# Kernel optimization log

Hardware: AMD Instinct MI355X
Metric: run time of the kernel (lower is better)

## Reference

```python
import jax, jax.numpy as jnp
import numpy as np

D_MODEL = 1024
NHEAD = 16
HEAD_DIM = D_MODEL // NHEAD
ROPE_BASE = 10000.0


def _rope_freq(T, head_dim):
    half = head_dim // 2
    pos = jnp.arange(T, dtype=jnp.float32)
    idx = jnp.arange(half, dtype=jnp.float32)
    freq_div = ROPE_BASE ** (2.0 * idx / head_dim)
    return pos[:, None] / freq_div[None, :]  # [T, half]


def _rope_rotate(x, cos, sin):
    # x: [B, H, T, d]; cos/sin: [T, d//2]
    half = x.shape[-1] // 2
    xl, xr = x[..., :half], x[..., half:]
    c = cos[None, None]
    s = sin[None, None]
    return jnp.concatenate([xl * c - xr * s, xl * s + xr * c], axis=-1)


def setup_inputs() -> dict:
    key = jax.random.key(0)
    ks = jax.random.split(key, 12)
    B, T = 2, 2048
    sd = 1.0 / np.sqrt(D_MODEL)
    inp = {
        "query": jax.random.normal(ks[0], (B, T, D_MODEL), jnp.float32),
        "key": jax.random.normal(ks[1], (B, T, D_MODEL), jnp.float32),
        "value": jax.random.normal(ks[2], (B, T, D_MODEL), jnp.float32),
        "frac": jax.random.uniform(ks[3], (B, T), jnp.float32),
        # Linear weights stored [in, out] (torch W.T)
        "Wq": jax.random.normal(ks[4], (D_MODEL, D_MODEL), jnp.float32) * sd,
        "Wk": jax.random.normal(ks[5], (D_MODEL, D_MODEL), jnp.float32) * sd,
        "Wv": jax.random.normal(ks[6], (D_MODEL, D_MODEL), jnp.float32) * sd,
        "Wo": jax.random.normal(ks[7], (D_MODEL, D_MODEL), jnp.float32) * sd,
        "bq": jnp.zeros((D_MODEL,), jnp.float32),
        "bk": jnp.zeros((D_MODEL,), jnp.float32),
        "bv": jnp.zeros((D_MODEL,), jnp.float32),
        "bo": jnp.zeros((D_MODEL,), jnp.float32),
        "alpha_pos": jax.random.normal(ks[8], (NHEAD,), jnp.float32) * 0.1,
        "alpha_neg": jax.random.normal(ks[9], (NHEAD,), jnp.float32) * 0.1,
    }
    return inp


def reference(query, key, value, frac, Wq, Wk, Wv, Wo, bq, bk, bv, bo, alpha_pos, alpha_neg):
    B, T, dm = query.shape
    H, hd = NHEAD, HEAD_DIM
    scale = hd ** -0.5

    def split_heads(x):  # [B,T,dm] -> [B,H,T,hd]
        return x.reshape(B, T, H, hd).transpose(0, 2, 1, 3)

    Q = split_heads(query @ Wq + bq)
    K = split_heads(key @ Wk + bk)
    V = split_heads(value @ Wv + bv)

    freq = _rope_freq(T, hd)
    cos, sin = jnp.cos(freq), jnp.sin(freq)
    Q = _rope_rotate(Q, cos, sin)
    K = _rope_rotate(K, cos, sin)

    scores = jnp.einsum("bhqd,bhkd->bhqk", Q, K) * scale  # [B,H,T,T]

    # data-dependent stoichiometric bias
    D = frac[:, None, :] - frac[:, :, None]  # [B,T,T], D[b,i,j] = frac_j - frac_i
    D_pos = jax.nn.relu(D)
    D_neg = -jax.nn.relu(-D)
    bias = (alpha_pos[None, :, None, None] * D_pos[:, None] +
            alpha_neg[None, :, None, None] * D_neg[:, None])  # [B,H,T,T]
    scores = scores + bias

    probs = jax.nn.softmax(scores, axis=-1)
    out = jnp.einsum("bhqk,bhkd->bhqd", probs, V)  # [B,H,T,hd]
    out = out.transpose(0, 2, 1, 3).reshape(B, T, dm)
    return out @ Wo + bo
```

## Files before the change

kernel.cpp:

```cpp
#include <hip/hip_runtime.h>


typedef unsigned short u16;
typedef __bf16 bf8v __attribute__((ext_vector_type(8)));
typedef __bf16 bf4v __attribute__((ext_vector_type(4)));
typedef float f32x4 __attribute__((ext_vector_type(4)));

#define D_MODEL 1024
#define T_SEQ   2048
#define NHEAD   16
#define HDIM    64
#define BATCH   2
#define M_TOT   (BATCH * T_SEQ)
#define LOG2E   1.4426950408889634f

__device__ __forceinline__ void gl2lds16(const u16* g, u16* l) {
  __builtin_amdgcn_global_load_lds(
      (__attribute__((address_space(1))) void*)g,
      (__attribute__((address_space(3))) void*)l, 16, 0, 0);
}

__global__ __launch_bounds__(256) void k_prep(
    const float* __restrict__ q, const float* __restrict__ k,
    const float* __restrict__ v, const float* __restrict__ Wq,
    const float* __restrict__ Wk, const float* __restrict__ Wv,
    const float* __restrict__ Wo, u16* __restrict__ Xb, u16* __restrict__ WtB,
    float* __restrict__ ct, float* __restrict__ st) {
  __shared__ float tile[64 * 65];
  int bx = blockIdx.x, tid = threadIdx.x;
  if (bx < 6144) {
    int z = bx >> 11, xb = bx & 2047;
    const float* src = (z == 0) ? q : (z == 1) ? k : v;
    u16* dst = Xb + (size_t)z * (M_TOT * D_MODEL);
    int idx = (xb * 256 + tid) * 8;
    float4 a = *(const float4*)(src + idx);
    float4 b = *(const float4*)(src + idx + 4);
    bf8v o;
    o[0] = (__bf16)a.x; o[1] = (__bf16)a.y; o[2] = (__bf16)a.z; o[3] = (__bf16)a.w;
    o[4] = (__bf16)b.x; o[5] = (__bf16)b.y; o[6] = (__bf16)b.z; o[7] = (__bf16)b.w;
    *(bf8v*)(dst + idx) = o;
  } else if (bx < 7168) {
    int idx2 = bx - 6144;
    int z = idx2 >> 8, rem = idx2 & 255;
    int k0 = (rem >> 4) * 64, n0 = (rem & 15) * 64;
    const float* W = (z == 0) ? Wq : (z == 1) ? Wk : (z == 2) ? Wv : Wo;
    u16* Wt = WtB + (size_t)z * (D_MODEL * D_MODEL);
#pragma unroll
    for (int i = 0; i < 16; i++) {
      int idx = tid + i * 256;
      int r = idx >> 6, c = idx & 63;
      tile[c * 65 + r] = W[(size_t)(k0 + r) * D_MODEL + n0 + c];
    }
    __syncthreads();
#pragma unroll
    for (int i = 0; i < 16; i++) {
      int idx = tid + i * 256;
      int r = idx >> 6, c = idx & 63;
      ((__bf16*)Wt)[(size_t)(n0 + r) * D_MODEL + k0 + c] = (__bf16)tile[r * 65 + c];
    }
  } else {
    int idx = (bx - 7168) * 256 + tid;
    int t = idx >> 5, d = idx & 31;
    float ang = (float)t * powf(10000.0f, -(float)d * (1.0f / 32.0f));
    ct[idx] = cosf(ang);
    st[idx] = sinf(ang);
  }
}

__device__ __forceinline__ void gemm_core_128(const u16* __restrict__ A,
                                              const u16* __restrict__ Bt,
                                              u16* sA, u16* sB,
                                              f32x4 (&acc)[4][4],
                                              int m0, int n0) {
  const int K = D_MODEL;
  int tid = threadIdx.x;
  int lane = tid & 63, wave = tid >> 6;
  int l15 = lane & 15, quad = lane >> 4;
  int wm = (wave >> 1) * 64, wn = (wave & 1) * 64;
  int r0 = tid >> 2, pcol0 = (tid & 3) * 8;
  int r1 = 64 + r0;
  const u16* A0 = A + (size_t)(m0 + r0) * K + pcol0;
  const u16* A1 = A + (size_t)(m0 + r1) * K + pcol0;
  const u16* B0 = Bt + (size_t)(n0 + r0) * K + pcol0;
  const u16* B1 = Bt + (size_t)(n0 + r1) * K + pcol0;
  u16* dA0 = sA + wave * 512;
  u16* dA1 = sA + 2048 + wave * 512;
  u16* dB0 = sB + wave * 512;
  u16* dB1 = sB + 2048 + wave * 512;
  for (int k0 = 0; k0 < K; k0 += 64) {
    __syncthreads();
    gl2lds16(A0 + k0, dA0);
    gl2lds16(A1 + k0, dA1);
    gl2lds16(A0 + k0 + 32, dA0 + 4096);
    gl2lds16(A1 + k0 + 32, dA1 + 4096);
    gl2lds16(B0 + k0, dB0);
    gl2lds16(B0 + k0 + 32, dB0 + 4096);
    gl2lds16(B1 + k0, dB1);
    gl2lds16(B1 + k0 + 32, dB1 + 4096);
    __syncthreads();
#pragma unroll
    for (int kh = 0; kh < 2; kh++) {
      bf8v af[4], bf[4];
#pragma unroll
      for (int i = 0; i < 4; i++)
        af[i] = *(const bf8v*)(sA + kh * 4096 + (wm + i * 16 + l15) * 32 + quad * 8);
#pragma unroll
      for (int i = 0; i < 4; i++)
        bf[i] = *(const bf8v*)(sB + kh * 4096 + (wn + i * 16 + l15) * 32 + quad * 8);
#pragma unroll
      for (int mi = 0; mi < 4; mi++)
#pragma unroll
        for (int ni = 0; ni < 4; ni++)
          acc[mi][ni] = __builtin_amdgcn_mfma_f32_16x16x32_bf16(
              af[mi], bf[ni], acc[mi][ni], 0, 0, 0);
    }
  }
}

__global__ __launch_bounds__(256) void k_gemm_qkv(
    const u16* __restrict__ Xb, const u16* __restrict__ WtB,
    const float* __restrict__ bq, const float* __restrict__ bk,
    const float* __restrict__ bv, const float* __restrict__ ctab,
    const float* __restrict__ stab, u16* __restrict__ OutB,
    u16* __restrict__ Vb) {
  __shared__ __align__(16) u16 sA[128 * 64];
  __shared__ __align__(16) u16 sB[128 * 64];
  int z = blockIdx.z;
  const u16* A = Xb + (size_t)z * (M_TOT * D_MODEL);
  const u16* Bt = WtB + (size_t)z * (D_MODEL * D_MODEL);
  const float* bias = (z == 0) ? bq : (z == 1) ? bk : bv;
  u16* Out = OutB + (size_t)z * (M_TOT * D_MODEL);
  int m0 = blockIdx.y * 128, n0 = blockIdx.x * 128;
  f32x4 acc[4][4] = {};
  gemm_core_128(A, Bt, sA, sB, acc, m0, n0);

  int tid = threadIdx.x, lane = tid & 63, wave = tid >> 6;
  int l15 = lane & 15, quad = lane >> 4;
  int wm = (wave >> 1) * 64, wn = (wave & 1) * 64;
  float bvv[4];
#pragma unroll
  for (int ni = 0; ni < 4; ni++) bvv[ni] = bias[n0 + wn + ni * 16 + l15];

  if (z < 2) {
    float qs = (z == 0) ? 0.125f * LOG2E : 1.0f;
#pragma unroll
    for (int mi = 0; mi < 4; mi++) {
#pragma unroll
      for (int r = 0; r < 4; r++) {
        int m = m0 + wm + mi * 16 + quad * 4 + r;
        size_t ro = (size_t)m * D_MODEL + n0 + wn;
        int tl = m & (T_SEQ - 1);
#pragma unroll
        for (int ni = 0; ni < 2; ni++) {
          int d = ni * 16 + l15;
          float c = ctab[tl * 32 + d], s = stab[tl * 32 + d];
          float xl = acc[mi][ni][r] + bvv[ni];
          float xr = acc[mi][ni + 2][r] + bvv[ni + 2];
          ((__bf16*)Out)[ro + d] = (__bf16)((xl * c - xr * s) * qs);
          ((__bf16*)Out)[ro + d + 32] = (__bf16)((xl * s + xr * c) * qs);
        }
      }
    }
  } else {
    int hh = (n0 + wn) >> 6;
    int mbase = m0 + wm;
    int bb = mbase >> 11;
    int tbase = mbase & (T_SEQ - 1);
    u16* Vw = Vb + (size_t)(bb * NHEAD + hh) * HDIM * T_SEQ;
#pragma unroll
    for (int mi = 0; mi < 4; mi++)
#pragma unroll
      for (int r = 0; r < 4; r++) {
        int t = tbase + mi * 16 + quad * 4 + r;
#pragma unroll
        for (int ni = 0; ni < 4; ni++) {
          int d = ni * 16 + l15;
          ((__bf16*)Vw)[(size_t)d * T_SEQ + t] = (__bf16)(acc[mi][ni][r] + bvv[ni]);
        }
      }
  }
}

__global__ __launch_bounds__(256) void k_gemm_out(
    const u16* __restrict__ ctx, const u16* __restrict__ Wot,
    const float* __restrict__ bo, float* __restrict__ Cout) {
  __shared__ __align__(16) u16 sA[64 * 64];
  __shared__ __align__(16) u16 sB[64 * 64];
  const int K = D_MODEL;
  int m0 = blockIdx.y * 64, n0 = blockIdx.x * 64;
  int tid = threadIdx.x, lane = tid & 63, wave = tid >> 6;
  int l15 = lane & 15, quad = lane >> 4;
  int wm = (wave >> 1) * 32, wn = (wave & 1) * 32;
  int r0 = tid >> 2, pcol0 = (tid & 3) * 8;
  const u16* A0 = ctx + (size_t)(m0 + r0) * K + pcol0;
  const u16* B0 = Wot + (size_t)(n0 + r0) * K + pcol0;
  u16* dA = sA + wave * 512;
  u16* dB = sB + wave * 512;
  f32x4 acc[2][2] = {};
  for (int k0 = 0; k0 < K; k0 += 64) {
    __syncthreads();
    gl2lds16(A0 + k0, dA);
    gl2lds16(A0 + k0 + 32, dA + 2048);
    gl2lds16(B0 + k0, dB);
    gl2lds16(B0 + k0 + 32, dB + 2048);
    __syncthreads();
#pragma unroll
    for (int kh = 0; kh < 2; kh++) {
      bf8v af[2], bf[2];
#pragma unroll
      for (int i = 0; i < 2; i++)
        af[i] = *(const bf8v*)(sA + kh * 2048 + (wm + i * 16 + l15) * 32 + quad * 8);
#pragma unroll
      for (int i = 0; i < 2; i++)
        bf[i] = *(const bf8v*)(sB + kh * 2048 + (wn + i * 16 + l15) * 32 + quad * 8);
#pragma unroll
      for (int mi = 0; mi < 2; mi++)
#pragma unroll
        for (int ni = 0; ni < 2; ni++)
          acc[mi][ni] = __builtin_amdgcn_mfma_f32_16x16x32_bf16(
              af[mi], bf[ni], acc[mi][ni], 0, 0, 0);
    }
  }
  float bvv[2];
#pragma unroll
  for (int ni = 0; ni < 2; ni++) bvv[ni] = bo[n0 + wn + ni * 16 + l15];
#pragma unroll
  for (int mi = 0; mi < 2; mi++)
#pragma unroll
    for (int r = 0; r < 4; r++) {
      size_t ro = (size_t)(m0 + wm + mi * 16 + quad * 4 + r) * D_MODEL + n0 + wn;
#pragma unroll
      for (int ni = 0; ni < 2; ni++)
        Cout[ro + ni * 16 + l15] = acc[mi][ni][r] + bvv[ni];
    }
}

__global__ __launch_bounds__(512, 4) void k_attn(
    const u16* __restrict__ Qr, const u16* __restrict__ Kr,
    const u16* __restrict__ Vb, const float* __restrict__ frac,
    const float* __restrict__ alpha_pos, const float* __restrict__ alpha_neg,
    u16* __restrict__ ctx) {
  __shared__ __align__(16) u16 smem[38912];
  int lin = blockIdx.x + (blockIdx.y << 4);
  int xcd = lin & 7, slot = lin >> 3;
  int bh = (xcd << 2) | (slot >> 4);
  int q0 = (slot & 15) << 7;
  int b = bh >> 4, h = bh & 15;
  int tid = threadIdx.x, wave = tid >> 6, lane = tid & 63;
  int l15 = lane & 15, quad = lane >> 4;
  int qw = wave & 3;
  int kh = wave >> 2;

  const u16* Kh = Kr + (size_t)b * T_SEQ * D_MODEL + h * HDIM;
  const u16* Vh = Vb + (size_t)bh * HDIM * T_SEQ;
  const float* fb = frac + b * T_SEQ;

  u16* kT0 = smem;
  u16* vT0 = smem + 12288;
  u16* pw = smem + 24576 + wave * 1280;
  float* fl = (float*)(smem + 34816);

  bf8v qf[2][2];
  float fq[2];
#pragma unroll
  for (int g = 0; g < 2; g++) {
    int qrow = q0 + qw * 32 + g * 16 + l15;
    const u16* qbase =
        Qr + (size_t)(b * T_SEQ + qrow) * D_MODEL + h * HDIM + quad * 8;
    qf[g][0] = *(const bf8v*)qbase;
    qf[g][1] = *(const bf8v*)(qbase + 32);
    fq[g] = fb[qrow];
  }
  {
    f32x4 fv = *(const f32x4*)(fb + (tid << 2));
    *(f32x4*)(fl + (tid << 2)) = fv;
  }

  float ap = alpha_pos[h] * LOG2E, an = alpha_neg[h] * LOG2E;
  float c1 = 0.5f * (ap + an), c2 = 0.5f * (ap - an);
  bf8v onesv;
#pragma unroll
  for (int j = 0; j < 8; j++) onesv[j] = (__bf16)1.0f;
  f32x4 o[2][4] = {};
  f32x4 o_l[2] = {};

  int x0 = (quad ^ (l15 & 7)) * 8;
  int kidx[2], vidx[4];
#pragma unroll
  for (int nt = 0; nt < 2; nt++)
    kidx[nt] = (((kh * 2 + nt) * 16 + l15) << 6) + x0;
#pragma unroll
  for (int dt = 0; dt < 4; dt++)
    vidx[dt] = (((dt * 16 + l15) << 6) + x0) ^ (kh * 32);
  int pidx = l15 * 40 + quad * 8;

  int kr0 = tid >> 3, gc0 = (tid & 7) ^ (kr0 & 7);
  const u16* kg0 = Kh + (size_t)kr0 * D_MODEL + gc0 * 8;
  const u16* vg0 = Vh + (size_t)kr0 * T_SEQ + gc0 * 8;
  int woff = wave * 512;

  auto stage = [&](int bufoff, int kbase) {
    gl2lds16(kg0 + (size_t)kbase * D_MODEL, kT0 + bufoff + woff);
    gl2lds16(vg0 + kbase, vT0 + bufoff + woff);
  };

  stage(0, 0);
  stage(4096, 64);
  asm volatile("s_waitcnt lgkmcnt(0)" ::: "memory");

  int oc = 0, o1 = 4096, o2 = 8192;
  for (int kt = 0; kt < T_SEQ / 64; kt++) {
    int kbase = kt * 64;
    if (kt == T_SEQ / 64 - 1)
      asm volatile("s_waitcnt vmcnt(0)" ::: "memory");
    else
      asm volatile("s_waitcnt vmcnt(2)" ::: "memory");
    __builtin_amdgcn_s_barrier();
    asm volatile("" ::: "memory");
    __builtin_amdgcn_sched_barrier(0);
    if (kt + 2 < T_SEQ / 64) stage(o2, kbase + 128);
    const u16* kb = kT0 + oc;
    const u16* vb = vT0 + oc;

    bf8v kf0[2], kf1[2];
#pragma unroll
    for (int nt = 0; nt < 2; nt++) {
      kf0[nt] = *(const bf8v*)(kb + kidx[nt]);
      kf1[nt] = *(const bf8v*)(kb + (kidx[nt] ^ 32));
    }
    bf8v vf[4];
#pragma unroll
    for (int dt = 0; dt < 4; dt++) vf[dt] = *(const bf8v*)(vb + vidx[dt]);
    f32x4 fk4[2];
#pragma unroll
    for (int nt = 0; nt < 2; nt++)
      fk4[nt] = *(const f32x4*)(fl + kbase + kh * 32 + nt * 16 + quad * 4);

#pragma unroll
    for (int g = 0; g < 2; g++) {
      float fqg = fq[g];
      u16* pwg = pw + g * 640;
#pragma unroll
      for (int nt = 0; nt < 2; nt++) {
        f32x4 s = {};
        __builtin_amdgcn_s_setprio(1);
        s = __builtin_amdgcn_mfma_f32_16x16x32_bf16(kf0[nt], qf[g][0], s, 0, 0, 0);
        s = __builtin_amdgcn_mfma_f32_16x16x32_bf16(kf1[nt], qf[g][1], s, 0, 0, 0);
        __builtin_amdgcn_s_setprio(0);
        bf4v pk;
#pragma unroll
        for (int r = 0; r < 4; r++) {
          float dd = fk4[nt][r] - fqg;
          pk[r] = (__bf16)__builtin_amdgcn_exp2f(
              fmaf(c2, __builtin_fabsf(dd), fmaf(c1, dd, s[r])));
        }
        *(bf4v*)(pwg + l15 * 40 + nt * 16 + quad * 4) = pk;
      }
      asm volatile("s_waitcnt lgkmcnt(0)" ::: "memory");
      bf8v pf = *(const bf8v*)(pwg + pidx);
      __builtin_amdgcn_s_setprio(1);
      o_l[g] = __builtin_amdgcn_mfma_f32_16x16x32_bf16(pf, onesv, o_l[g], 0, 0, 0);
#pragma unroll
      for (int dt = 0; dt < 4; dt++)
        o[g][dt] = __builtin_amdgcn_mfma_f32_16x16x32_bf16(pf, vf[dt],
                                                           o[g][dt], 0, 0, 0);
      __builtin_amdgcn_s_setprio(0);
    }
    int tmp = oc; oc = o1; o1 = o2; o2 = tmp;
  }
  __syncthreads();

  float* Of = (float*)smem;
  float* Lf = (float*)(smem + 16896);
  if (kh == 1) {
#pragma unroll
    for (int g = 0; g < 2; g++)
#pragma unroll
      for (int r = 0; r < 4; r++) {
        int ql = qw * 32 + g * 16 + quad * 4 + r;
#pragma unroll
        for (int dt = 0; dt < 4; dt++)
          Of[ql * 66 + dt * 16 + l15] = o[g][dt][r];
        if (l15 == 0) Lf[ql] = o_l[g][r];
      }
  }
  __syncthreads();
  if (kh == 0) {
#pragma unroll
    for (int g = 0; g < 2; g++)
#pragma unroll
      for (int r = 0; r < 4; r++) {
        int ql = qw * 32 + g * 16 + quad * 4 + r;
        float linv = 1.0f / (o_l[g][r] + Lf[ql]);
        __bf16* orow =
            (__bf16*)(ctx + (size_t)(b * T_SEQ + q0 + ql) * D_MODEL + h * HDIM);
#pragma unroll
        for (int dt = 0; dt < 4; dt++)
          orow[dt * 16 + l15] =
              (__bf16)((o[g][dt][r] + Of[ql * 66 + dt * 16 + l15]) * linv);
      }
  }
}

extern "C" void kernel_launch(void* const* d_in, const int* in_sizes, int n_in,
                              void* d_out, int out_size, void* d_ws,
                              size_t ws_size, hipStream_t stream) {
  const float* q = (const float*)d_in[0];
  const float* k = (const float*)d_in[1];
  const float* v = (const float*)d_in[2];
  const float* frac = (const float*)d_in[3];
  const float* Wq = (const float*)d_in[4];
  const float* Wk = (const float*)d_in[5];
  const float* Wv = (const float*)d_in[6];
  const float* Wo = (const float*)d_in[7];
  const float* bq = (const float*)d_in[8];
  const float* bk = (const float*)d_in[9];
  const float* bv = (const float*)d_in[10];
  const float* bo = (const float*)d_in[11];
  const float* alpha_pos = (const float*)d_in[12];
  const float* alpha_neg = (const float*)d_in[13];

  char* ws = (char*)d_ws;
  u16* Xb = (u16*)(ws + 0);
  u16* Wt = (u16*)(ws + 25165824);
  u16* Qr = (u16*)(ws + 33554432);
  u16* Kr = (u16*)(ws + 41943040);
  u16* Vtmp = (u16*)(ws + 50331648);
  u16* Vb = (u16*)(ws + 58720256);
  float* ctab = (float*)(ws + 67108864);
  float* stab = (float*)(ws + 67371008);
  u16* ctx = Vtmp;
  u16* QKVout = Qr;

  k_prep<<<dim3(7424), 256, 0, stream>>>(q, k, v, Wq, Wk, Wv, Wo, Xb, Wt, ctab,
                                         stab);
  k_gemm_qkv<<<dim3(8, 32, 3), 256, 0, stream>>>(Xb, Wt, bq, bk, bv, ctab, stab,
                                                 QKVout, Vb);
  k_attn<<<dim3(16, 32), 512, 0, stream>>>(Qr, Kr, Vb, frac, alpha_pos,
                                           alpha_neg, ctx);
  k_gemm_out<<<dim3(16, 64), 256, 0, stream>>>(ctx, Wt + 3 * 1048576, bo,
                                               (float*)d_out);
}
```

Measured before the change: 238.0 us.

## Transpose attention probabilities in registers via permlane swaps and shrink LDS buffering

Result: faster. 231.6 us (-2.7%).

```diff
diff --git a/kernel.cpp b/kernel.cpp
--- a/kernel.cpp
+++ b/kernel.cpp
@@ -5,6 +5,7 @@
 typedef __bf16 bf8v __attribute__((ext_vector_type(8)));
 typedef __bf16 bf4v __attribute__((ext_vector_type(4)));
 typedef float f32x4 __attribute__((ext_vector_type(4)));
+typedef unsigned int u32x4v __attribute__((ext_vector_type(4)));
 
 #define D_MODEL 1024
 #define T_SEQ   2048
@@ -240,7 +241,7 @@
     const u16* __restrict__ Vb, const float* __restrict__ frac,
     const float* __restrict__ alpha_pos, const float* __restrict__ alpha_neg,
     u16* __restrict__ ctx) {
-  __shared__ __align__(16) u16 smem[38912];
+  __shared__ __align__(16) u16 smem[20480];
   int lin = blockIdx.x + (blockIdx.y << 4);
   int xcd = lin & 7, slot = lin >> 3;
   int bh = (xcd << 2) | (slot >> 4);
@@ -256,9 +257,8 @@
   const float* fb = frac + b * T_SEQ;
 
   u16* kT0 = smem;
-  u16* vT0 = smem + 12288;
-  u16* pw = smem + 24576 + wave * 1280;
-  float* fl = (float*)(smem + 34816);
+  u16* vT0 = smem + 8192;
+  float* fl = (float*)(smem + 16384);
 
   bf8v qf[2][2];
   float fq[2];
@@ -281,6 +281,7 @@
   bf8v onesv;
 #pragma unroll
   for (int j = 0; j < 8; j++) onesv[j] = (__bf16)1.0f;
+  f32x4 zero4 = {};
   f32x4 o[2][4] = {};
   f32x4 o_l[2] = {};
 
@@ -292,7 +293,6 @@
 #pragma unroll
   for (int dt = 0; dt < 4; dt++)
     vidx[dt] = (((dt * 16 + l15) << 6) + x0) ^ (kh * 32);
-  int pidx = l15 * 40 + quad * 8;
 
   int kr0 = tid >> 3, gc0 = (tid & 7) ^ (kr0 & 7);
   const u16* kg0 = Kh + (size_t)kr0 * D_MODEL + gc0 * 8;
@@ -305,22 +305,15 @@
   };
 
   stage(0, 0);
-  stage(4096, 64);
-  asm volatile("s_waitcnt lgkmcnt(0)" ::: "memory");
-
-  int oc = 0, o1 = 4096, o2 = 8192;
+  __syncthreads();
+
+#pragma unroll 2
   for (int kt = 0; kt < T_SEQ / 64; kt++) {
     int kbase = kt * 64;
-    if (kt == T_SEQ / 64 - 1)
-      asm volatile("s_waitcnt vmcnt(0)" ::: "memory");
-    else
-      asm volatile("s_waitcnt vmcnt(2)" ::: "memory");
-    __builtin_amdgcn_s_barrier();
-    asm volatile("" ::: "memory");
-    __builtin_amdgcn_sched_barrier(0);
-    if (kt + 2 < T_SEQ / 64) stage(o2, kbase + 128);
-    const u16* kb = kT0 + oc;
-    const u16* vb = vT0 + oc;
+    int bo = (kt & 1) * 4096;
+    if (kt + 1 < T_SEQ / 64) stage(bo ^ 4096, kbase + 64);
+    const u16* kb = kT0 + bo;
+    const u16* vb = vT0 + bo;
 
     bf8v kf0[2], kf1[2];
 #pragma unroll
@@ -339,36 +332,40 @@
 #pragma unroll
     for (int g = 0; g < 2; g++) {
       float fqg = fq[g];
-      u16* pwg = pw + g * 640;
+      unsigned int wrd[4];
 #pragma unroll
       for (int nt = 0; nt < 2; nt++) {
-        f32x4 s = {};
-        __builtin_amdgcn_s_setprio(1);
+        f32x4 s = zero4;
         s = __builtin_amdgcn_mfma_f32_16x16x32_bf16(kf0[nt], qf[g][0], s, 0, 0, 0);
         s = __builtin_amdgcn_mfma_f32_16x16x32_bf16(kf1[nt], qf[g][1], s, 0, 0, 0);
-        __builtin_amdgcn_s_setprio(0);
-        bf4v pk;
+        float p[4];
 #pragma unroll
         for (int r = 0; r < 4; r++) {
           float dd = fk4[nt][r] - fqg;
-          pk[r] = (__bf16)__builtin_amdgcn_exp2f(
+          p[r] = __builtin_amdgcn_exp2f(
               fmaf(c2, __builtin_fabsf(dd), fmaf(c1, dd, s[r])));
         }
-        *(bf4v*)(pwg + l15 * 40 + nt * 16 + quad * 4) = pk;
+        unsigned int w0, w1;
+        asm("v_cvt_pk_bf16_f32 %0, %1, %2" : "=v"(w0) : "v"(p[0]), "v"(p[1]));
+        asm("v_cvt_pk_bf16_f32 %0, %1, %2" : "=v"(w1) : "v"(p[2]), "v"(p[3]));
+        wrd[nt * 2 + 0] = w0;
+        wrd[nt * 2 + 1] = w1;
       }
-      asm volatile("s_waitcnt lgkmcnt(0)" ::: "memory");
-      bf8v pf = *(const bf8v*)(pwg + pidx);
-      __builtin_amdgcn_s_setprio(1);
+      asm("v_permlane32_swap_b32 %0, %1" : "+v"(wrd[0]), "+v"(wrd[2]));
+      asm("v_permlane16_swap_b32 %0, %1" : "+v"(wrd[0]), "+v"(wrd[2]));
+      asm("v_permlane32_swap_b32 %0, %1" : "+v"(wrd[1]), "+v"(wrd[3]));
+      asm("v_permlane16_swap_b32 %0, %1" : "+v"(wrd[1]), "+v"(wrd[3]));
+      u32x4v pw_;
+      pw_.x = wrd[0]; pw_.y = wrd[1]; pw_.z = wrd[2]; pw_.w = wrd[3];
+      bf8v pf = __builtin_bit_cast(bf8v, pw_);
       o_l[g] = __builtin_amdgcn_mfma_f32_16x16x32_bf16(pf, onesv, o_l[g], 0, 0, 0);
 #pragma unroll
       for (int dt = 0; dt < 4; dt++)
         o[g][dt] = __builtin_amdgcn_mfma_f32_16x16x32_bf16(pf, vf[dt],
                                                            o[g][dt], 0, 0, 0);
-      __builtin_amdgcn_s_setprio(0);
-    }
-    int tmp = oc; oc = o1; o1 = o2; o2 = tmp;
-  }
-  __syncthreads();
+    }
+    __syncthreads();
+  }
 
   float* Of = (float*)smem;
   float* Lf = (float*)(smem + 16896);
```
